# Optimization experiments

Hardware: AMD Instinct MI355X
Metric: run time of the kernel (lower is better)

## Reference

```python
import jax, jax.numpy as jnp
import numpy as np

L, B, D, H = 2048, 2, 1024, 16


def setup_inputs() -> dict:
    key = jax.random.key(0)
    ks = jax.random.split(key, 4)
    x = jax.random.normal(ks[0], (L, B, D), dtype=jnp.float32)
    W_in = jax.random.normal(ks[1], (3 * D, D), dtype=jnp.float32) * (1.0 / np.sqrt(D))
    b_in = jnp.zeros((3 * D,), dtype=jnp.float32)
    W_out = jax.random.normal(ks[2], (D, D), dtype=jnp.float32) * (1.0 / np.sqrt(D))
    b_out = jnp.zeros((D,), dtype=jnp.float32)
    mask = jnp.zeros((1, L, L), dtype=jnp.float32)
    return {"q": x, "k": x, "v": x, "mask": mask,
            "W_in": W_in, "b_in": b_in, "W_out": W_out, "b_out": b_out,
            "num_heads": H}


def reference(q, k, v, mask, W_in, b_in, W_out, b_out, num_heads):
    l, b, d = q.shape
    hd = d // num_heads
    # fused QKV projection (q == k == v in this module)
    qkv = q @ W_in.T + b_in                      # (l, b, 3d)
    qh, kh, vh = jnp.split(qkv, 3, axis=-1)      # each (l, b, d)

    def to_heads(t):
        # (l, b, d) -> (b*h, l, hd)
        return t.reshape(l, b * num_heads, hd).transpose(1, 0, 2)

    qh, kh, vh = to_heads(qh), to_heads(kh), to_heads(vh)
    qh = qh / jnp.sqrt(jnp.asarray(hd, dtype=qh.dtype))
    scores = jnp.einsum('nld,nmd->nlm', qh, kh) + mask   # (b*h, l, l)
    attn = jax.nn.softmax(scores, axis=-1)
    z = jnp.einsum('nlm,nmd->nld', attn, vh)             # (b*h, l, hd)
    z = z.transpose(1, 0, 2).reshape(l * b, d)
    z = z @ W_out.T + b_out
    return z.reshape(l, b, d)
```

## Files before the change

kernel.cpp:

```cpp
#include <hip/hip_runtime.h>


typedef short  s8v  __attribute__((ext_vector_type(8)));
typedef short  s4vv __attribute__((ext_vector_type(4)));
typedef float  f4v  __attribute__((ext_vector_type(4)));
typedef float  f4l  __attribute__((ext_vector_type(4)));
typedef float  f16v __attribute__((ext_vector_type(16)));
typedef int    i4v  __attribute__((ext_vector_type(4)));
typedef int    i2v  __attribute__((ext_vector_type(2)));

__device__ __forceinline__ short f2bf(float f) {
  union { float f; unsigned u; } x; x.f = f;
  unsigned r = (x.u + 0x7fffu + ((x.u >> 16) & 1u)) >> 16;
  return (short)r;
}

__device__ __forceinline__ int cvtpk(float lo, float hi) {
  int r;
  asm("v_cvt_pk_bf16_f32 %0, %1, %2" : "=v"(r) : "v"(lo), "v"(hi));
  return r;
}

#define GLDS16(gp, lp) __builtin_amdgcn_global_load_lds( \
    (const __attribute__((address_space(1))) void*)(gp),  \
    (__attribute__((address_space(3))) void*)(lp), 16, 0, 0)

#define LOG2E 1.4426950408889634f

__global__ __launch_bounds__(256) void prep(const float* __restrict__ x,
                                            const float* __restrict__ wi,
                                            const float* __restrict__ wo,
                                            const float* __restrict__ mask,
                                            short* __restrict__ xb,
                                            short* __restrict__ wib,
                                            short* __restrict__ wob,
                                            unsigned* __restrict__ flags) {
  const int b = blockIdx.x;
  if (b < 8192) {
    int i = b * 256 + threadIdx.x;
    const float* src; short* dst; int off;
    if (i < 1048576)               { src = x;  dst = xb;  off = i; }
    else if (i < 1048576 + 786432) { src = wi; dst = wib; off = i - 1048576; }
    else                           { src = wo; dst = wob; off = i - 1835008; }
    f4l v = ((const f4l*)src)[off];
    s4vv o;
    o[0] = f2bf(v[0]); o[1] = f2bf(v[1]); o[2] = f2bf(v[2]); o[3] = f2bf(v[3]);
    ((s4vv*)dst)[off] = o;
  } else {
    const int l = b - 8192;
    const int qt = l >> 7;
    const int t = threadIdx.x;
    const float* row = mask + ((size_t)l << 11) + (t << 3);
    f4l a = *(const f4l*)row;
    f4l bb = *(const f4l*)(row + 4);
    bool nz = (a[0] != 0.f) | (a[1] != 0.f) | (a[2] != 0.f) | (a[3] != 0.f) |
              (bb[0] != 0.f) | (bb[1] != 0.f) | (bb[2] != 0.f) | (bb[3] != 0.f);
    unsigned long long bal = __ballot(nz);
    const int w = t >> 6, lane = t & 63;
    if (lane == 0 && bal) {
      unsigned bits = 0;
#pragma unroll
      for (int g = 0; g < 8; ++g)
        if ((bal >> (g << 3)) & 0xFFull) bits |= 1u << ((w << 3) + g);
      atomicOr(&flags[qt], bits);
    }
  }
}

__global__ __launch_bounds__(256) void gemm_qkv(const short* __restrict__ A,
                                                const short* __restrict__ B,
                                                const float* __restrict__ bin,
                                                short* __restrict__ Qh,
                                                short* __restrict__ Kh,
                                                short* __restrict__ VT) {
  __shared__ __align__(16) short As[128 * 64];
  __shared__ __align__(16) short Bs[128 * 64];
  const int tid = threadIdx.x;
  const int w = tid >> 6, lane = tid & 63;
  const int g = lane >> 4, c15 = lane & 15;
  const int wr = w >> 1, wc = w & 1;
  const int rowbase = blockIdx.y << 7;
  const int colbase = blockIdx.x << 7;
  const int rl = lane >> 3, sp = lane & 7;
  const int swz = (sp ^ rl) << 3;

  f4v acc[4][4] = {};

  for (int kt = 0; kt < 16; ++kt) {
#pragma unroll
    for (int c2 = 0; c2 < 4; ++c2) {
      const int chunk = (w << 2) + c2;
      const int row = (chunk << 3) + rl;
      GLDS16(A + ((size_t)(rowbase + row) << 10) + (kt << 6) + swz, &As[chunk << 9]);
      GLDS16(B + ((size_t)(colbase + row) << 10) + (kt << 6) + swz, &Bs[chunk << 9]);
    }
    __syncthreads();
#pragma unroll
    for (int kk = 0; kk < 2; ++kk) {
      s8v af[4], bf[4];
#pragma unroll
      for (int m = 0; m < 4; ++m) {
        const int row = (wr << 6) + (m << 4) + c15;
        af[m] = *(const s8v*)((const char*)As + row * 128 + ((((kk << 2) | g) ^ (row & 7)) << 4));
        const int col = (wc << 6) + (m << 4) + c15;
        bf[m] = *(const s8v*)((const char*)Bs + col * 128 + ((((kk << 2) | g) ^ (col & 7)) << 4));
      }
#pragma unroll
      for (int m = 0; m < 4; ++m)
#pragma unroll
        for (int nn = 0; nn < 4; ++nn)
          acc[m][nn] = __builtin_amdgcn_mfma_f32_16x16x32_bf16(af[m], bf[nn], acc[m][nn], 0, 0, 0);
    }
    __syncthreads();
  }

  const int r0 = rowbase + (wr << 6) + (g << 2);
  const int c0 = colbase + (wc << 6) + c15;
  const int which = colbase >> 10;
#pragma unroll
  for (int nn = 0; nn < 4; ++nn) {
    const int col = c0 + (nn << 4);
    const int dd = col & 1023;
    const int hh = dd >> 6, ee = dd & 63;
    const float bias = bin[col];
    if (which == 2) {
      unsigned* v0p = (unsigned*)(VT + ((((size_t)hh << 6) + ee) << 11));
      unsigned* v1p = (unsigned*)(VT + (((((size_t)hh + 16) << 6) + ee) << 11));
#pragma unroll
      for (int m = 0; m < 4; ++m) {
        const int li0 = (r0 >> 1) + (m << 3);
        v0p[li0 >> 1] = (unsigned)cvtpk(acc[m][nn][0] + bias, acc[m][nn][2] + bias);
        v1p[li0 >> 1] = (unsigned)cvtpk(acc[m][nn][1] + bias, acc[m][nn][3] + bias);
      }
    } else {
      const float mul = (which == 0) ? 0.125f * LOG2E : 1.0f;
      short* dst = (which == 0) ? Qh : Kh;
#pragma unroll
      for (int m = 0; m < 4; ++m) {
#pragma unroll
        for (int j = 0; j < 4; ++j) {
          const int row = r0 + (m << 4) + j;
          const int li = row >> 1, bb = row & 1;
          const int nh = (bb << 4) + hh;
          dst[(((size_t)nh * 2048 + li) << 6) + ee] = f2bf((acc[m][nn][j] + bias) * mul);
        }
      }
    }
  }
}

__global__ __launch_bounds__(256) void gemm_out(const short* __restrict__ A,
                                                const short* __restrict__ B,
                                                const float* __restrict__ bout,
                                                float* __restrict__ out) {
  __shared__ __align__(16) short As[128 * 64];
  __shared__ __align__(16) short Bs[128 * 64];
  const int tid = threadIdx.x;
  const int w = tid >> 6, lane = tid & 63;
  const int g = lane >> 4, c15 = lane & 15;
  const int wr = w >> 1, wc = w & 1;
  const int rowbase = blockIdx.y << 7;
  const int colbase = blockIdx.x << 7;
  const int rl = lane >> 3, sp = lane & 7;
  const int swz = (sp ^ rl) << 3;

  f4v acc[4][4] = {};

  for (int kt = 0; kt < 16; ++kt) {
#pragma unroll
    for (int c2 = 0; c2 < 4; ++c2) {
      const int chunk = (w << 2) + c2;
      const int row = (chunk << 3) + rl;
      GLDS16(A + ((size_t)(rowbase + row) << 10) + (kt << 6) + swz, &As[chunk << 9]);
      GLDS16(B + ((size_t)(colbase + row) << 10) + (kt << 6) + swz, &Bs[chunk << 9]);
    }
    __syncthreads();
#pragma unroll
    for (int kk = 0; kk < 2; ++kk) {
      s8v af[4], bf[4];
#pragma unroll
      for (int m = 0; m < 4; ++m) {
        const int row = (wr << 6) + (m << 4) + c15;
        af[m] = *(const s8v*)((const char*)As + row * 128 + ((((kk << 2) | g) ^ (row & 7)) << 4));
        const int col = (wc << 6) + (m << 4) + c15;
        bf[m] = *(const s8v*)((const char*)Bs + col * 128 + ((((kk << 2) | g) ^ (col & 7)) << 4));
      }
#pragma unroll
      for (int m = 0; m < 4; ++m)
#pragma unroll
        for (int nn = 0; nn < 4; ++nn)
          acc[m][nn] = __builtin_amdgcn_mfma_f32_16x16x32_bf16(af[m], bf[nn], acc[m][nn], 0, 0, 0);
    }
    __syncthreads();
  }

  const int r0 = rowbase + (wr << 6) + (g << 2);
  const int c0 = colbase + (wc << 6) + c15;
#pragma unroll
  for (int nn = 0; nn < 4; ++nn) {
    const int col = c0 + (nn << 4);
    const float bias = bout[col];
#pragma unroll
    for (int m = 0; m < 4; ++m) {
#pragma unroll
      for (int j = 0; j < 4; ++j) {
        const int row = r0 + (m << 4) + j;
        out[((size_t)row << 10) + col] = acc[m][nn][j] + bias;
      }
    }
  }
}

__global__ __launch_bounds__(256, 2) void attn(const short* __restrict__ Qh,
                                               const short* __restrict__ Kh,
                                               const short* __restrict__ VTg,
                                               const float* __restrict__ mask,
                                               const unsigned* __restrict__ mflags,
                                               short* __restrict__ Z) {
  __shared__ __align__(16) short Ks[3][64 * 64];
  __shared__ __align__(16) short Vs[3][64 * 64];
  const int tid = threadIdx.x;
  const int w = tid >> 6, lane = tid & 63;
  const int q5 = lane & 31, hi = lane >> 5;
  const int orig = blockIdx.x;
  const int wg = ((orig & 7) << 6) + (orig >> 3);
  const int n = wg >> 4, qt = wg & 15;
  const int srow8 = lane >> 3, sp = lane & 7;
  const int ssw = (sp ^ srow8) << 3;

  const int qg = (qt << 7) + (w << 5) + q5;

  const short* Qp = Qh + (((size_t)n * 2048 + qg) << 6);
  s8v bq[4];
#pragma unroll
  for (int ks = 0; ks < 4; ++ks)
    bq[ks] = *(const s8v*)(Qp + (ks << 4) + (hi << 3));

  const short* Kbase = Kh + ((size_t)n << 17);
  const short* Vbase = VTg + ((size_t)n << 17);
  const float* mrow = mask + ((size_t)qg << 11) + (hi << 2);
  const unsigned mbits = mflags[qt];
  const int kslot = q5 & 7;

  f16v oA0, oA1, zz;
#pragma unroll
  for (int e = 0; e < 16; ++e) { oA0[e] = 0.0f; oA1[e] = 0.0f; zz[e] = 0.0f; }
  float ls0 = 0.0f, ls1 = 0.0f;

#define VMW(N) asm volatile("s_waitcnt vmcnt(" #N ")" ::: "memory")
#define BAR()  do { __builtin_amdgcn_s_barrier(); asm volatile("" ::: "memory"); } while (0)

#define STAGEK(bi, t) do { const int cw = w << 1;                               \
    GLDS16(Kbase + ((size_t)(((t) << 6) + (cw << 3) + srow8) << 6) + ssw,       \
           &Ks[bi][cw << 9]);                                                   \
    GLDS16(Kbase + ((size_t)(((t) << 6) + ((cw + 1) << 3) + srow8) << 6) + ssw, \
           &Ks[bi][(cw + 1) << 9]); } while (0)
#define STAGEV(bi, t) do { const int cw = w << 1;                               \
    GLDS16(Vbase + ((size_t)((cw << 3) + srow8) << 11) + ((t) << 6) + ssw,      \
           &Vs[bi][cw << 9]);                                                   \
    GLDS16(Vbase + ((size_t)(((cw + 1) << 3) + srow8) << 11) + ((t) << 6) + ssw,\
           &Vs[bi][(cw + 1) << 9]); } while (0)

#define QKM(S0_, S1_, bi) do {                                                  \
    const char* Kc = (const char*)&Ks[bi][0];                                   \
    __builtin_amdgcn_s_setprio(1);                                              \
    _Pragma("unroll")                                                           \
    for (int ks = 0; ks < 4; ++ks) {                                            \
      const int so = ((2 * ks + hi) ^ kslot) << 4;                              \
      s8v ak0 = *(const s8v*)(Kc + q5 * 128 + so);                              \
      s8v ak1 = *(const s8v*)(Kc + (q5 + 32) * 128 + so);                       \
      if (ks == 0) {                                                            \
        S0_ = __builtin_amdgcn_mfma_f32_32x32x16_bf16(ak0, bq[0], zz, 0, 0, 0); \
        S1_ = __builtin_amdgcn_mfma_f32_32x32x16_bf16(ak1, bq[0], zz, 0, 0, 0); \
      } else {                                                                  \
        S0_ = __builtin_amdgcn_mfma_f32_32x32x16_bf16(ak0, bq[ks], S0_, 0,0,0); \
        S1_ = __builtin_amdgcn_mfma_f32_32x32x16_bf16(ak1, bq[ks], S1_, 0,0,0); \
      } }                                                                       \
    __builtin_amdgcn_s_setprio(0); } while (0)

#define SMPV(S0_, S1_, t, bi) do {                                              \
    if ((mbits >> (t)) & 1u) {                                                  \
      const float* mp = mrow + ((t) << 6);                                      \
      _Pragma("unroll")                                                         \
      for (int c = 0; c < 4; ++c) {                                             \
        f4l mv0 = *(const f4l*)(mp + (c << 3));                                 \
        f4l mv1 = *(const f4l*)(mp + 32 + (c << 3));                            \
        _Pragma("unroll")                                                       \
        for (int j = 0; j < 4; ++j) {                                           \
          S0_[(c << 2) + j] += mv0[j] * LOG2E;                                  \
          S1_[(c << 2) + j] += mv1[j] * LOG2E;                                  \
        } } }                                                                   \
    _Pragma("unroll")                                                           \
    for (int r = 0; r < 16; ++r) {                                              \
      float a = __builtin_amdgcn_exp2f(S0_[r]); S0_[r] = a; ls0 += a;           \
      float b = __builtin_amdgcn_exp2f(S1_[r]); S1_[r] = b; ls1 += b;           \
    }                                                                           \
    const char* Vc = (const char*)&Vs[bi][0];                                   \
    __builtin_amdgcn_s_setprio(1);                                              \
    _Pragma("unroll")                                                           \
    for (int ks = 0; ks < 4; ++ks) {                                            \
      const f16v& sv = (ks < 2) ? S0_ : S1_;                                    \
      const int ro = (ks & 1) << 3;                                             \
      int P0 = cvtpk(sv[ro + 0], sv[ro + 1]);                                   \
      int P1 = cvtpk(sv[ro + 2], sv[ro + 3]);                                   \
      int P2 = cvtpk(sv[ro + 4], sv[ro + 5]);                                   \
      int P3 = cvtpk(sv[ro + 6], sv[ro + 7]);                                   \
      int x0 = __shfl_xor(P2, 32);                                              \
      int x1 = __shfl_xor(P3, 32);                                              \
      int x2 = __shfl_xor(P0, 32);                                              \
      int x3 = __shfl_xor(P1, 32);                                              \
      union { i4v i; s8v s; } pu;                                               \
      pu.i[0] = hi ? x0 : P0;                                                   \
      pu.i[1] = hi ? x1 : P1;                                                   \
      pu.i[2] = hi ? P2 : x2;                                                   \
      pu.i[3] = hi ? P3 : x3;                                                   \
      const int so = ((2 * ks + hi) ^ kslot) << 4;                              \
      s8v av0 = *(const s8v*)(Vc + q5 * 128 + so);                              \
      s8v av1 = *(const s8v*)(Vc + (q5 + 32) * 128 + so);                       \
      oA0 = __builtin_amdgcn_mfma_f32_32x32x16_bf16(av0, pu.s, oA0, 0, 0, 0);   \
      oA1 = __builtin_amdgcn_mfma_f32_32x32x16_bf16(av1, pu.s, oA1, 0, 0, 0);   \
    }                                                                           \
    __builtin_amdgcn_s_setprio(0); } while (0)

  f16v sA0, sA1, sB0, sB1;

  asm volatile("s_waitcnt vmcnt(0)" ::: "memory");
  STAGEK(0, 0); STAGEV(0, 0); STAGEK(1, 1); STAGEV(1, 1); STAGEK(2, 2);
  VMW(8);
  BAR();
  QKM(sA0, sA1, 0);
  VMW(4);
  BAR();

  int bc = 0;
  for (int p = 0; p < 28; p += 2) {
    const int b1 = (bc == 2) ? 0 : bc + 1;
    const int b2 = (b1 == 2) ? 0 : b1 + 1;
    STAGEK(bc, p + 3);
    STAGEV(b2, p + 2);
    QKM(sB0, sB1, b1);
    SMPV(sA0, sA1, p, bc);
    VMW(4); BAR();
    STAGEK(b1, p + 4);
    STAGEV(bc, p + 3);
    QKM(sA0, sA1, b2);
    SMPV(sB0, sB1, p + 1, b1);
    VMW(4); BAR();
    bc = b2;
  }
  STAGEK(1, 31);
  STAGEV(0, 30);
  QKM(sB0, sB1, 2);
  SMPV(sA0, sA1, 28, 1);
  VMW(4); BAR();
  STAGEV(1, 31);
  QKM(sA0, sA1, 0);
  SMPV(sB0, sB1, 29, 2);
  VMW(2); BAR();
  QKM(sB0, sB1, 1);
  SMPV(sA0, sA1, 30, 0);
  VMW(0); BAR();
  SMPV(sB0, sB1, 31, 1);

#undef STAGEK
#undef STAGEV
#undef QKM
#undef SMPV
#undef VMW
#undef BAR

  float lrun = ls0 + ls1;
  lrun += __shfl_xor(lrun, 32);
  const float invl = 1.0f / lrun;
  short* zp = Z + ((((size_t)qg << 1) + (n >> 4)) << 10) + ((n & 15) << 6);
#pragma unroll
  for (int c = 0; c < 4; ++c) {
    const int d0 = (c << 3) + (hi << 2);
    i2v w0, w1;
    w0[0] = cvtpk(oA0[(c << 2) + 0] * invl, oA0[(c << 2) + 1] * invl);
    w0[1] = cvtpk(oA0[(c << 2) + 2] * invl, oA0[(c << 2) + 3] * invl);
    *(i2v*)(zp + d0) = w0;
    w1[0] = cvtpk(oA1[(c << 2) + 0] * invl, oA1[(c << 2) + 1] * invl);
    w1[1] = cvtpk(oA1[(c << 2) + 2] * invl, oA1[(c << 2) + 3] * invl);
    *(i2v*)(zp + 32 + d0) = w1;
  }
}

extern "C" void kernel_launch(void* const* d_in, const int* in_sizes, int n_in,
                              void* d_out, int out_size, void* d_ws, size_t ws_size,
                              hipStream_t stream) {
  const float* xq   = (const float*)d_in[0];
  const float* mask = (const float*)d_in[3];
  const float* Win  = (const float*)d_in[4];
  const float* bin  = (const float*)d_in[5];
  const float* Wout = (const float*)d_in[6];
  const float* bout = (const float*)d_in[7];
  float* out = (float*)d_out;

  char* ws = (char*)d_ws;
  short* xb  = (short*)(ws);
  short* wib = (short*)(ws + (8ull  << 20));
  short* wob = (short*)(ws + (14ull << 20));
  short* Qh  = (short*)(ws + (16ull << 20));
  short* Kh  = (short*)(ws + (24ull << 20));
  short* VTg = (short*)(ws + (32ull << 20));
  short* Zb  = (short*)(ws + (40ull << 20));
  unsigned* mflags = (unsigned*)(ws + (48ull << 20));

  hipMemsetAsync(mflags, 0, 16 * sizeof(unsigned), stream);
  prep<<<8192 + 2048, 256, 0, stream>>>(xq, Win, Wout, mask, xb, wib, wob, mflags);
  gemm_qkv<<<dim3(24, 32), 256, 0, stream>>>(xb, wib, bin, Qh, Kh, VTg);
  attn<<<512, 256, 0, stream>>>(Qh, Kh, VTg, mask, mflags, Zb);
  gemm_out<<<dim3(8, 32), 256, 0, stream>>>(Zb, wob, bout, out);
}
```

Measured before the change: 138.6 us.

## Remap GEMM blocks per XCD for L2 locality and halve output GEMM tile width

Both GEMMs now use a 1D grid and remap block IDs so that blocks landing on the same XCD (round-robin by blockIdx mod 8) share contiguous row/column tiles, improving L2 reuse of A and B operands. The output GEMM also switches from 128x128 to 128x64 tiles, doubling the block count from 256 to 512 to better fill the 256 CUs. Smaller tiles reduce per-block arithmetic intensity and increase redundant A loads.

New measurement: 134.1 us. -3.2%, faster.

```diff
diff --git a/kernel.cpp b/kernel.cpp
--- a/kernel.cpp
+++ b/kernel.cpp
@@ -79,8 +79,12 @@
   const int w = tid >> 6, lane = tid & 63;
   const int g = lane >> 4, c15 = lane & 15;
   const int wr = w >> 1, wc = w & 1;
-  const int rowbase = blockIdx.y << 7;
-  const int colbase = blockIdx.x << 7;
+  const int orig = blockIdx.x;
+  const int xcd = orig & 7, j6 = orig >> 3;
+  const int bx = ((xcd & 1) * 12) + (j6 % 12);
+  const int by = ((xcd >> 1) * 8) + (j6 / 12);
+  const int rowbase = by << 7;
+  const int colbase = bx << 7;
   const int rl = lane >> 3, sp = lane & 7;
   const int swz = (sp ^ rl) << 3;
 
@@ -154,17 +158,20 @@
                                                 const float* __restrict__ bout,
                                                 float* __restrict__ out) {
   __shared__ __align__(16) short As[128 * 64];
-  __shared__ __align__(16) short Bs[128 * 64];
+  __shared__ __align__(16) short Bs[64 * 64];
   const int tid = threadIdx.x;
   const int w = tid >> 6, lane = tid & 63;
   const int g = lane >> 4, c15 = lane & 15;
-  const int wr = w >> 1, wc = w & 1;
-  const int rowbase = blockIdx.y << 7;
-  const int colbase = blockIdx.x << 7;
+  const int orig = blockIdx.x;
+  const int xcd = orig & 7, j6 = orig >> 3;
+  const int colblk = (xcd << 1) + (j6 & 1);
+  const int rowblk = j6 >> 1;
+  const int rowbase = rowblk << 7;
+  const int colbase = colblk << 6;
   const int rl = lane >> 3, sp = lane & 7;
   const int swz = (sp ^ rl) << 3;
 
-  f4v acc[4][4] = {};
+  f4v acc[2][4] = {};
 
   for (int kt = 0; kt < 16; ++kt) {
 #pragma unroll
@@ -172,21 +179,29 @@
       const int chunk = (w << 2) + c2;
       const int row = (chunk << 3) + rl;
       GLDS16(A + ((size_t)(rowbase + row) << 10) + (kt << 6) + swz, &As[chunk << 9]);
+    }
+#pragma unroll
+    for (int c2 = 0; c2 < 2; ++c2) {
+      const int chunk = (w << 1) + c2;
+      const int row = (chunk << 3) + rl;
       GLDS16(B + ((size_t)(colbase + row) << 10) + (kt << 6) + swz, &Bs[chunk << 9]);
     }
     __syncthreads();
 #pragma unroll
     for (int kk = 0; kk < 2; ++kk) {
-      s8v af[4], bf[4];
-#pragma unroll
-      for (int m = 0; m < 4; ++m) {
-        const int row = (wr << 6) + (m << 4) + c15;
+      s8v af[2], bf[4];
+#pragma unroll
+      for (int m = 0; m < 2; ++m) {
+        const int row = (w << 5) + (m << 4) + c15;
         af[m] = *(const s8v*)((const char*)As + row * 128 + ((((kk << 2) | g) ^ (row & 7)) << 4));
-        const int col = (wc << 6) + (m << 4) + c15;
-        bf[m] = *(const s8v*)((const char*)Bs + col * 128 + ((((kk << 2) | g) ^ (col & 7)) << 4));
-      }
-#pragma unroll
-      for (int m = 0; m < 4; ++m)
+      }
+#pragma unroll
+      for (int nn = 0; nn < 4; ++nn) {
+        const int col = (nn << 4) + c15;
+        bf[nn] = *(const s8v*)((const char*)Bs + col * 128 + ((((kk << 2) | g) ^ (col & 7)) << 4));
+      }
+#pragma unroll
+      for (int m = 0; m < 2; ++m)
 #pragma unroll
         for (int nn = 0; nn < 4; ++nn)
           acc[m][nn] = __builtin_amdgcn_mfma_f32_16x16x32_bf16(af[m], bf[nn], acc[m][nn], 0, 0, 0);
@@ -194,14 +209,14 @@
     __syncthreads();
   }
 
-  const int r0 = rowbase + (wr << 6) + (g << 2);
-  const int c0 = colbase + (wc << 6) + c15;
+  const int r0 = rowbase + (w << 5) + (g << 2);
+  const int c0 = colbase + c15;
 #pragma unroll
   for (int nn = 0; nn < 4; ++nn) {
     const int col = c0 + (nn << 4);
     const float bias = bout[col];
 #pragma unroll
-    for (int m = 0; m < 4; ++m) {
+    for (int m = 0; m < 2; ++m) {
 #pragma unroll
       for (int j = 0; j < 4; ++j) {
         const int row = r0 + (m << 4) + j;
@@ -409,7 +424,7 @@
 
   hipMemsetAsync(mflags, 0, 16 * sizeof(unsigned), stream);
   prep<<<8192 + 2048, 256, 0, stream>>>(xq, Win, Wout, mask, xb, wib, wob, mflags);
-  gemm_qkv<<<dim3(24, 32), 256, 0, stream>>>(xb, wib, bin, Qh, Kh, VTg);
+  gemm_qkv<<<768, 256, 0, stream>>>(xb, wib, bin, Qh, Kh, VTg);
   attn<<<512, 256, 0, stream>>>(Qh, Kh, VTg, mask, mflags, Zb);
-  gemm_out<<<dim3(8, 32), 256, 0, stream>>>(Zb, wob, bout, out);
-}
+  gemm_out<<<512, 256, 0, stream>>>(Zb, wob, bout, out);
+}
```
